# Optimization experiments

Measured on AMD Instinct MI355X. Metric: run time of the kernel, lower is better.

Reference implementation:

```python
import jax, jax.numpy as jnp
import numpy as np

B, T, N, F = 4096, 64, 8, 4
H = 64           # GRU hidden
EID = 16         # id embedding dim
CM = 32          # comm message dim
D = H + EID + CM # 112, attention dim
INV_SQRT_D = 1.0 / np.sqrt(112.0)


def setup_inputs() -> dict:
    key = jax.random.key(0)
    ks = jax.random.split(key, 24)
    def rn(k, shape, s=0.05):
        return jax.random.normal(k, shape, jnp.float32) * s
    return {
        "seq": jax.random.normal(ks[0], (B, T, N, F), jnp.float32),
        # GRU (torch layout: W_ih [3H,F], W_hh [3H,H], gates ordered r,z,n)
        "W_ih": rn(ks[1], (3 * H, F)), "W_hh": rn(ks[2], (3 * H, H)),
        "b_ih": rn(ks[3], (3 * H,)), "b_hh": rn(ks[4], (3 * H,)),
        "embed": rn(ks[5], (8, EID)),
        "Wm": rn(ks[6], (CM, H + EID)), "bm": rn(ks[7], (CM,)),
        "Wq": rn(ks[8], (D, D)), "bq": rn(ks[9], (D,)),
        "Wk": rn(ks[10], (D, D)), "bk": rn(ks[11], (D,)),
        "Wv": rn(ks[12], (D, D)), "bv": rn(ks[13], (D,)),
        "W1": rn(ks[14], (128, D)), "b1": rn(ks[15], (128,)),
        "W2": rn(ks[16], (128, 128)), "b2": rn(ks[17], (128,)),
        "Wmean": rn(ks[18], (2, 128)), "bmean": rn(ks[19], (2,)),
        "Wval": rn(ks[20], (1, 128)), "bval": rn(ks[21], (1,)),
    }


def _policy(seq, W_ih, W_hh, b_ih, b_hh, embed, Wm, bm,
            Wq, bq, Wk, bk, Wv, bv, W1, b1, W2, b2, Wmean, bmean, Wval, bval):
    Bb, Tt, Nn, Ff = seq.shape
    # Faithful to torch: raw view [B,T,N,F] -> [B*N,T,F] (no permute)
    x = seq.reshape(Bb * Nn, Tt, Ff)
    # Precompute all input-to-hidden projections once: [BN, T, 3H]
    x_proj = jnp.einsum('btf,gf->btg', x, W_ih) + b_ih

    def step(h, xp):
        gh = h @ W_hh.T + b_hh
        xr, xz, xn = jnp.split(xp, 3, axis=-1)
        hr, hz, hn = jnp.split(gh, 3, axis=-1)
        r = jax.nn.sigmoid(xr + hr)
        z = jax.nn.sigmoid(xz + hz)
        n = jnp.tanh(xn + r * hn)
        return (1.0 - z) * n + z * h, None

    h0 = jnp.zeros((Bb * Nn, H), seq.dtype)
    hT, _ = jax.lax.scan(step, h0, jnp.swapaxes(x_proj, 0, 1))  # carry == out[:, -1]
    h = hT.reshape(Bb, Nn, H)

    id_emb = jnp.broadcast_to(embed[:Nn], (Bb, Nn, EID))
    msgs = jnp.concatenate([h, id_emb], axis=-1) @ Wm.T + bm      # [B,N,32]
    c = jnp.broadcast_to(msgs.mean(axis=1, keepdims=True), (Bb, Nn, CM))
    h = jnp.concatenate([h, id_emb, c], axis=-1)                   # [B,N,112]

    Q = h @ Wq.T + bq
    K = h @ Wk.T + bk
    V = h @ Wv.T + bv
    attn = jax.nn.softmax(jnp.einsum('bnd,bmd->bnm', Q, K) * INV_SQRT_D, axis=-1)
    h = jnp.einsum('bnm,bmd->bnd', attn, V)

    h = jax.nn.relu(h @ W1.T + b1)
    h = jax.nn.relu(h @ W2.T + b2)
    return (h @ Wmean.T + bmean, h @ Wval.T + bval)


def reference(seq, W_ih, W_hh, b_ih, b_hh, embed, Wm, bm,
              Wq, bq, Wk, bk, Wv, bv, W1, b1, W2, b2, Wmean, bmean, Wval, bval):
    return _policy(seq, W_ih, W_hh, b_ih, b_hh, embed, Wm, bm,
                   Wq, bq, Wk, bk, Wv, bv, W1, b1, W2, b2,
                   Wmean, bmean, Wval, bval)
```

## Files before the change

### kernel.cpp

```cpp
#include <hip/hip_runtime.h>


typedef float f32x4 __attribute__((ext_vector_type(4)));
typedef short bf16x8 __attribute__((ext_vector_type(8)));

#define MFMA16 __builtin_amdgcn_mfma_f32_16x16x32_bf16
#define LOG2E 1.44269504088896f
#define INV_SQRT_D 0.09449111825230679f

__device__ __forceinline__ short f2bf(float f) {
    union { float f; unsigned u; } v; v.f = f;
    unsigned r = v.u + 0x7fffu + ((v.u >> 16) & 1u);
    return (short)(r >> 16);
}
__device__ __forceinline__ short f2bf_hu(float f) {
    union { float f; unsigned u; } v; v.f = f;
    return (short)((v.u + 0x8000u) >> 16);
}
__device__ __forceinline__ float fexp2(float x) { return __builtin_amdgcn_exp2f(x); }
__device__ __forceinline__ float frcp(float x)  { return __builtin_amdgcn_rcpf(x); }

__global__ void conv_kernel(
    const float* __restrict__ Wm, const float* __restrict__ Wq,
    const float* __restrict__ Wk, const float* __restrict__ Wv,
    const float* __restrict__ W1, const float* __restrict__ W2,
    const float* __restrict__ Wmean, const float* __restrict__ Wval,
    unsigned short* __restrict__ wf)
{
    int gid = blockIdx.x * 256 + threadIdx.x;
    if (gid >= 158 * 64) return;
    int fid = gid >> 6, lane = gid & 63;
    int l15 = lane & 15, q = lane >> 4;

    short out[8] = {0,0,0,0,0,0,0,0};
    if (fid < 154) {
        const float* W; int nrows, Klim, idx;
        if (fid < 6)        { W = Wm; nrows = 32;  Klim = 80;  idx = fid;       }
        else if (fid < 34)  { W = Wq; nrows = 112; Klim = 112; idx = fid - 6;   }
        else if (fid < 62)  { W = Wk; nrows = 112; Klim = 112; idx = fid - 34;  }
        else if (fid < 90)  { W = Wv; nrows = 112; Klim = 112; idx = fid - 62;  }
        else if (fid < 122) { W = W1; nrows = 128; Klim = 112; idx = fid - 90;  }
        else                { W = W2; nrows = 128; Klim = 128; idx = fid - 122; }
        int nch = (fid < 6) ? 3 : 4;
        int ct = idx / nch, ch = idx - ct * nch;
        int g = ct * 16 + l15, k0 = ch * 32 + q * 8;
        if (g < nrows && (k0 + 8) <= Klim) {
            const float* wp = W + (size_t)g * Klim + k0;
            #pragma unroll
            for (int u = 0; u < 8; ++u) out[u] = f2bf(wp[u]);
        }
    } else {
        int ch = fid - 154, k0 = ch * 32 + q * 8;
        const float* wp = (l15 == 0) ? Wmean : (l15 == 1) ? (Wmean + 128)
                          : (l15 == 2) ? Wval : nullptr;
        if (wp) {
            #pragma unroll
            for (int u = 0; u < 8; ++u) out[u] = f2bf(wp[k0 + u]);
        }
    }
    *(bf16x8*)(wf + ((size_t)fid * 64 + lane) * 8) = *(bf16x8*)out;
}

__global__ __launch_bounds__(256, 2) void gru_kernel(
    const float* __restrict__ seq,
    const float* __restrict__ W_ih,
    const float* __restrict__ W_hh,
    const float* __restrict__ b_ih,
    const float* __restrict__ b_hh,
    unsigned short* __restrict__ h_out)
{
    __shared__ short hlds[4][16][72];
    const int tid  = threadIdx.x;
    const int wave = tid >> 6;
    const int lane = tid & 63;
    const int l15  = lane & 15;
    const int q    = lane >> 4;
    const int seqbase = (blockIdx.x * 4 + wave) * 16;
    short (*hl)[72] = hlds[wave];

    {
        int* p = (int*)&hl[0][0];
        #pragma unroll
        for (int i = 0; i < 9; ++i) p[lane + 64 * i] = 0;
    }

    const float sc_rz = -LOG2E;
    const float sc_n  = 2.0f * LOG2E;

    bf16x8 Bh[12][2];
    bf16x8 B2[12];
    bf16x8 B2x[4];
    #pragma unroll
    for (int j = 0; j < 12; ++j) {
        int g = j * 16 + l15;
        float s = (j < 8) ? sc_rz : sc_n;
        #pragma unroll
        for (int c = 0; c < 2; ++c) {
            const float* wp = W_hh + g * 64 + c * 32 + q * 8;
            bf16x8 f;
            #pragma unroll
            for (int u = 0; u < 8; ++u) f[u] = f2bf(wp[u] * s);
            Bh[j][c] = f;
        }
        bf16x8 f2 = {0,0,0,0,0,0,0,0};
        if (q == 0) {
            if (j < 8) {
                #pragma unroll
                for (int u = 0; u < 4; ++u) f2[u] = f2bf(W_ih[g * 4 + u] * s);
                f2[4] = f2bf((b_ih[g] + b_hh[g]) * s);
            } else {
                f2[4] = f2bf(b_hh[g] * s);
            }
        }
        B2[j] = f2;
    }
    #pragma unroll
    for (int j2 = 0; j2 < 4; ++j2) {
        int g = 128 + j2 * 16 + l15;
        bf16x8 f = {0,0,0,0,0,0,0,0};
        if (q == 0) {
            #pragma unroll
            for (int u = 0; u < 4; ++u) f[u] = f2bf(W_ih[g * 4 + u] * sc_n);
            f[4] = f2bf(b_ih[g] * sc_n);
        }
        B2x[j2] = f;
    }

    const short onebf = 0x3f80;
    float h[4][4];
    #pragma unroll
    for (int j = 0; j < 4; ++j)
        #pragma unroll
        for (int r = 0; r < 4; ++r) h[j][r] = 0.f;

    f32x4 xc = *(const f32x4*)(seq + (size_t)(seqbase + l15) * 256);
    const f32x4 zz = {0.f, 0.f, 0.f, 0.f};

    for (int t = 0; t < 64; ++t) {
        f32x4 xnext;
        if (t < 63)
            xnext = *(const f32x4*)(seq + (size_t)(seqbase + l15) * 256 + (t + 1) * 4);

        bf16x8 A0 = *(const bf16x8*)&hl[l15][q * 8];
        bf16x8 A1 = *(const bf16x8*)&hl[l15][32 + q * 8];
        bf16x8 A2;
        A2[0] = f2bf_hu(xc[0]); A2[1] = f2bf_hu(xc[1]);
        A2[2] = f2bf_hu(xc[2]); A2[3] = f2bf_hu(xc[3]);
        A2[4] = onebf; A2[5] = 0; A2[6] = 0; A2[7] = 0;

        #pragma unroll
        for (int j = 0; j < 4; ++j) {
            f32x4 ar = MFMA16(A2, B2[j], zz, 0, 0, 0);
            ar = MFMA16(A0, Bh[j][0], ar, 0, 0, 0);
            ar = MFMA16(A1, Bh[j][1], ar, 0, 0, 0);
            f32x4 az = MFMA16(A2, B2[4 + j], zz, 0, 0, 0);
            az = MFMA16(A0, Bh[4 + j][0], az, 0, 0, 0);
            az = MFMA16(A1, Bh[4 + j][1], az, 0, 0, 0);
            f32x4 an = MFMA16(A2, B2[8 + j], zz, 0, 0, 0);
            an = MFMA16(A0, Bh[8 + j][0], an, 0, 0, 0);
            an = MFMA16(A1, Bh[8 + j][1], an, 0, 0, 0);
            f32x4 ax = MFMA16(A2, B2x[j], zz, 0, 0, 0);

            #pragma unroll
            for (int r = 0; r < 4; ++r) {
                float e_r  = fexp2(ar[r]);
                float rg   = frcp(1.f + e_r);
                float e_z  = fexp2(az[r]);
                float npre = fmaf(rg, an[r], ax[r]);
                float e_t  = fexp2(npre);
                float tp   = e_t + 1.f;
                float tm   = e_t - 1.f;
                float hv   = h[j][r];
                float num  = fmaf(hv, tp, e_z * tm);
                float den  = tp * (1.f + e_z);
                float hnew = num * frcp(den);
                h[j][r] = hnew;
                hl[q * 4 + r][16 * j + l15] = f2bf_hu(hnew);
            }
        }
        if (t < 63) xc = xnext;
    }

    #pragma unroll
    for (int j = 0; j < 4; ++j)
        #pragma unroll
        for (int r = 0; r < 4; ++r)
            h_out[(size_t)(seqbase + q * 4 + r) * 64 + 16 * j + l15] =
                (unsigned short)f2bf_hu(h[j][r]);
}

__global__ __launch_bounds__(256, 2) void head_kernel(
    const unsigned short* __restrict__ hseq,
    const unsigned short* __restrict__ wf,
    const float* __restrict__ embed,
    const float* __restrict__ bm, const float* __restrict__ bq,
    const float* __restrict__ bk, const float* __restrict__ bv,
    const float* __restrict__ b1, const float* __restrict__ b2,
    const float* __restrict__ bmean, const float* __restrict__ bval,
    float* __restrict__ out)
{
    __shared__ short R1[64][136];
    __shared__ short R2[64][136];
    __shared__ short R3[64][136];
    __shared__ short Vt[112][80];
    __shared__ short Pb[64][40];

    float (*msgs)[33]  = (float(*)[33])&R3[0][0];
    float (*cmean)[32] = (float(*)[32])&Pb[0][0];

    const int tid  = threadIdx.x;
    const int w    = tid >> 6;
    const int lane = tid & 63;
    const int l15  = lane & 15;
    const int q    = lane >> 4;
    const int agent0 = blockIdx.x * 64;
    const f32x4 zz4 = {0.f, 0.f, 0.f, 0.f};

    auto ld = [&](int fid) -> bf16x8 {
        return *(const bf16x8*)(wf + ((size_t)fid * 64 + lane) * 8);
    };

    {
        int* p;
        p = (int*)&R1[0][0]; for (int i = tid; i < 4352; i += 256) p[i] = 0;
        p = (int*)&R2[0][0]; for (int i = tid; i < 4352; i += 256) p[i] = 0;
        p = (int*)&Vt[0][0]; for (int i = tid; i < 4480; i += 256) p[i] = 0;
        p = (int*)&Pb[0][0]; for (int i = tid; i < 1280; i += 256) p[i] = 0;
    }
    __syncthreads();

    for (int i = tid; i < 512; i += 256) {
        int row = i >> 3, part = i & 7;
        *(bf16x8*)&R1[row][part * 8] =
            *(const bf16x8*)(hseq + (size_t)(agent0 + row) * 64 + part * 8);
    }
    for (int i = tid; i < 1024; i += 256) {
        int row = i >> 4, e = i & 15;
        R1[row][64 + e] = f2bf(embed[(row & 7) * 16 + e]);
    }
    __syncthreads();

    #pragma unroll
    for (int ct = 0; ct < 2; ++ct) {
        f32x4 acc = zz4;
        #pragma unroll
        for (int ch = 0; ch < 3; ++ch) {
            bf16x8 a = *(const bf16x8*)&R1[16 * w + l15][ch * 32 + q * 8];
            acc = MFMA16(a, ld(ct * 3 + ch), acc, 0, 0, 0);
        }
        float bias = bm[16 * ct + l15];
        #pragma unroll
        for (int r = 0; r < 4; ++r) msgs[16 * w + q * 4 + r][16 * ct + l15] = acc[r] + bias;
    }
    __syncthreads();

    {
        int b = tid >> 5, m = tid & 31;
        float s = 0.f;
        #pragma unroll
        for (int j = 0; j < 8; ++j) s += msgs[b * 8 + j][m];
        cmean[b][m] = 0.125f * s;
    }
    __syncthreads();
    for (int i = tid; i < 2048; i += 256) {
        int row = i >> 5, m = i & 31;
        R1[row][80 + m] = f2bf_hu(cmean[row >> 3][m]);
    }
    __syncthreads();

    for (int i = tid; i < 512; i += 256) {
        int row = i >> 3, cp = i & 7;
        *(int*)&R3[row][112 + cp * 2] = 0;
    }
    for (int i = tid; i < 768; i += 256) {
        int row = i / 12, cp = i - row * 12;
        *(int*)&Pb[row][16 + cp * 2] = 0;
    }
    #pragma unroll
    for (int ct = 0; ct < 7; ++ct) {
        f32x4 aq = zz4, ak = zz4, av = zz4;
        #pragma unroll
        for (int ch = 0; ch < 4; ++ch) {
            bf16x8 a = *(const bf16x8*)&R1[16 * w + l15][ch * 32 + q * 8];
            aq = MFMA16(a, ld(6  + ct * 4 + ch), aq, 0, 0, 0);
            ak = MFMA16(a, ld(34 + ct * 4 + ch), ak, 0, 0, 0);
            av = MFMA16(a, ld(62 + ct * 4 + ch), av, 0, 0, 0);
        }
        int col = 16 * ct + l15;
        float biq = bq[col], bik = bk[col], biv = bv[col];
        #pragma unroll
        for (int r = 0; r < 4; ++r) {
            int row = 16 * w + q * 4 + r;
            R2[row][col] = f2bf_hu((aq[r] + biq) * INV_SQRT_D);
            R3[row][col] = f2bf_hu(ak[r] + bik);
            Vt[col][row] = f2bf_hu(av[r] + biv);
        }
    }
    __syncthreads();

    {
        f32x4 acc = zz4;
        #pragma unroll
        for (int ch = 0; ch < 4; ++ch) {
            bf16x8 a = *(const bf16x8*)&R2[16 * w + l15][ch * 32 + q * 8];
            bf16x8 b = *(const bf16x8*)&R3[16 * w + l15][ch * 32 + q * 8];
            acc = MFMA16(a, b, acc, 0, 0, 0);
        }
        bool collow = (l15 < 8);
        #pragma unroll
        for (int r = 0; r < 4; ++r) {
            int rl = q * 4 + r;
            bool valid = ((rl < 8) == collow);
            float v = acc[r];
            float m = v;
            m = fmaxf(m, __shfl_xor(m, 1, 64));
            m = fmaxf(m, __shfl_xor(m, 2, 64));
            m = fmaxf(m, __shfl_xor(m, 4, 64));
            float e = fexp2(LOG2E * (v - m));
            float s = e;
            s += __shfl_xor(s, 1, 64);
            s += __shfl_xor(s, 2, 64);
            s += __shfl_xor(s, 4, 64);
            float pv = valid ? e * frcp(s) : 0.f;
            Pb[16 * w + rl][l15] = f2bf_hu(pv);
        }
    }
    __syncthreads();

    #pragma unroll
    for (int ct = 0; ct < 7; ++ct) {
        bf16x8 a = *(const bf16x8*)&Pb[16 * w + l15][q * 8];
        bf16x8 b = *(const bf16x8*)&Vt[16 * ct + l15][16 * w + q * 8];
        f32x4 acc = MFMA16(a, b, zz4, 0, 0, 0);
        #pragma unroll
        for (int r = 0; r < 4; ++r) R1[16 * w + q * 4 + r][16 * ct + l15] = f2bf_hu(acc[r]);
    }
    __syncthreads();

    #pragma unroll
    for (int ct = 0; ct < 8; ++ct) {
        f32x4 acc = zz4;
        #pragma unroll
        for (int ch = 0; ch < 4; ++ch) {
            bf16x8 a = *(const bf16x8*)&R1[16 * w + l15][ch * 32 + q * 8];
            acc = MFMA16(a, ld(90 + ct * 4 + ch), acc, 0, 0, 0);
        }
        float bias = b1[16 * ct + l15];
        #pragma unroll
        for (int r = 0; r < 4; ++r)
            R2[16 * w + q * 4 + r][16 * ct + l15] = f2bf_hu(fmaxf(acc[r] + bias, 0.f));
    }
    __syncthreads();

    #pragma unroll
    for (int ct = 0; ct < 8; ++ct) {
        f32x4 acc = zz4;
        #pragma unroll
        for (int ch = 0; ch < 4; ++ch) {
            bf16x8 a = *(const bf16x8*)&R2[16 * w + l15][ch * 32 + q * 8];
            acc = MFMA16(a, ld(122 + ct * 4 + ch), acc, 0, 0, 0);
        }
        float bias = b2[16 * ct + l15];
        #pragma unroll
        for (int r = 0; r < 4; ++r)
            R3[16 * w + q * 4 + r][16 * ct + l15] = f2bf_hu(fmaxf(acc[r] + bias, 0.f));
    }
    __syncthreads();

    {
        f32x4 acc = zz4;
        #pragma unroll
        for (int ch = 0; ch < 4; ++ch) {
            bf16x8 a = *(const bf16x8*)&R3[16 * w + l15][ch * 32 + q * 8];
            acc = MFMA16(a, ld(154 + ch), acc, 0, 0, 0);
        }
        if (l15 < 3) {
            float bias = (l15 == 0) ? bmean[0] : (l15 == 1) ? bmean[1] : bval[0];
            #pragma unroll
            for (int r = 0; r < 4; ++r) {
                int A = agent0 + 16 * w + q * 4 + r;
                float v = acc[r] + bias;
                if (l15 < 2) out[(size_t)A * 2 + l15] = v;
                else         out[65536 + A] = v;
            }
        }
    }
}

extern "C" void kernel_launch(void* const* d_in, const int* in_sizes, int n_in,
                              void* d_out, int out_size, void* d_ws, size_t ws_size,
                              hipStream_t stream) {
    const float* seq   = (const float*)d_in[0];
    const float* W_ih  = (const float*)d_in[1];
    const float* W_hh  = (const float*)d_in[2];
    const float* b_ih  = (const float*)d_in[3];
    const float* b_hh  = (const float*)d_in[4];
    const float* embed = (const float*)d_in[5];
    const float* Wm    = (const float*)d_in[6];
    const float* bm    = (const float*)d_in[7];
    const float* Wq    = (const float*)d_in[8];
    const float* bq    = (const float*)d_in[9];
    const float* Wk    = (const float*)d_in[10];
    const float* bk    = (const float*)d_in[11];
    const float* Wv    = (const float*)d_in[12];
    const float* bv    = (const float*)d_in[13];
    const float* W1    = (const float*)d_in[14];
    const float* b1    = (const float*)d_in[15];
    const float* W2    = (const float*)d_in[16];
    const float* b2    = (const float*)d_in[17];
    const float* Wmean = (const float*)d_in[18];
    const float* bmean = (const float*)d_in[19];
    const float* Wval  = (const float*)d_in[20];
    const float* bval  = (const float*)d_in[21];

    unsigned short* hbuf = (unsigned short*)d_ws;
    unsigned short* wf   = hbuf + (size_t)32768 * 64;

    conv_kernel<<<40, 256, 0, stream>>>(Wm, Wq, Wk, Wv, W1, W2, Wmean, Wval, wf);
    gru_kernel<<<512, 256, 0, stream>>>(seq, W_ih, W_hh, b_ih, b_hh, hbuf);
    head_kernel<<<512, 256, 0, stream>>>(hbuf, wf, embed, bm, bq, bk, bv,
                                         b1, b2, bmean, bval, (float*)d_out);
}
```

Baseline: 254.5 us.

## Fuse GRU and head into one per-wave kernel with LDS-only handoff

Merges the GRU recurrence and the attention/MLP head into a single kernel. Each wave keeps its 16 agents' final hidden state in its private LDS region and runs the head on them directly, which removes the global bf16 hidden-state round trip and one kernel launch. Block-wide __syncthreads are replaced by wave-local lgkmcnt waits, and the comm mean is computed with a shuffle reduction instead of a shared scratch pass. In exchange, per-block LDS grows, the head's weight-fragment loads now fall inside the long-latency GRU kernel, and the head work is serialized per wave after the recurrence.

```diff
diff --git a/kernel.cpp b/kernel.cpp
--- a/kernel.cpp
+++ b/kernel.cpp
@@ -19,6 +19,9 @@
 }
 __device__ __forceinline__ float fexp2(float x) { return __builtin_amdgcn_exp2f(x); }
 __device__ __forceinline__ float frcp(float x)  { return __builtin_amdgcn_rcpf(x); }
+__device__ __forceinline__ void lds_fence() {
+    __asm__ __volatile__("s_waitcnt lgkmcnt(0)" ::: "memory");
+}
 
 __global__ void conv_kernel(
     const float* __restrict__ Wm, const float* __restrict__ Wq,
@@ -50,7 +53,7 @@
             for (int u = 0; u < 8; ++u) out[u] = f2bf(wp[u]);
         }
     } else {
-        int ch = fid - 154, k0 = ch * 32 + q * 8;
+        int ch = fid - 154, k0 = ch * 32 + (lane >> 4) * 8;
         const float* wp = (l15 == 0) ? Wmean : (l15 == 1) ? (Wmean + 128)
                           : (l15 == 2) ? Wval : nullptr;
         if (wp) {
@@ -61,35 +64,56 @@
     *(bf16x8*)(wf + ((size_t)fid * 64 + lane) * 8) = *(bf16x8*)out;
 }
 
-__global__ __launch_bounds__(256, 2) void gru_kernel(
+__global__ __launch_bounds__(256, 2) void policy_kernel(
     const float* __restrict__ seq,
-    const float* __restrict__ W_ih,
-    const float* __restrict__ W_hh,
-    const float* __restrict__ b_ih,
-    const float* __restrict__ b_hh,
-    unsigned short* __restrict__ h_out)
+    const float* __restrict__ W_ih, const float* __restrict__ W_hh,
+    const float* __restrict__ b_ih, const float* __restrict__ b_hh,
+    const float* __restrict__ embed,
+    const unsigned short* __restrict__ wf,
+    const float* __restrict__ bm, const float* __restrict__ bq,
+    const float* __restrict__ bk, const float* __restrict__ bv,
+    const float* __restrict__ b1, const float* __restrict__ b2,
+    const float* __restrict__ bmean, const float* __restrict__ bval,
+    float* __restrict__ out)
 {
-    __shared__ short hlds[4][16][72];
+    __shared__ short R1s[4][16][136];
+    __shared__ short R2s[4][16][136];
+    __shared__ short R3s[4][16][136];
+    __shared__ short Vts[4][114][20];
+    __shared__ short Pbs[4][16][40];
+
     const int tid  = threadIdx.x;
-    const int wave = tid >> 6;
+    const int wv   = tid >> 6;
     const int lane = tid & 63;
     const int l15  = lane & 15;
     const int q    = lane >> 4;
-    const int seqbase = (blockIdx.x * 4 + wave) * 16;
-    short (*hl)[72] = hlds[wave];
-
-    {
-        int* p = (int*)&hl[0][0];
-        #pragma unroll
-        for (int i = 0; i < 9; ++i) p[lane + 64 * i] = 0;
+    const int seqbase = (blockIdx.x * 4 + wv) * 16;
+
+    short (*R1)[136] = R1s[wv];
+    short (*R2)[136] = R2s[wv];
+    short (*R3)[136] = R3s[wv];
+    short (*Vt)[20]  = Vts[wv];
+    short (*Pb)[40]  = Pbs[wv];
+    const f32x4 zz = {0.f, 0.f, 0.f, 0.f};
+
+    {
+        int* p;
+        p = (int*)&R1[0][0]; for (int i = lane; i < 1088; i += 64) p[i] = 0;
+        p = (int*)&R2[0][0]; for (int i = lane; i < 1088; i += 64) p[i] = 0;
+        p = (int*)&R3[0][0]; for (int i = lane; i < 1088; i += 64) p[i] = 0;
+        p = (int*)&Vt[0][0]; for (int i = lane; i < 1140; i += 64) p[i] = 0;
+        p = (int*)&Pb[0][0]; for (int i = lane; i < 320;  i += 64) p[i] = 0;
+    }
+    {
+        int row = lane >> 2, j0 = (lane & 3) * 4;
+        f32x4 e = *(const f32x4*)(embed + (row & 7) * 16 + j0);
+        #pragma unroll
+        for (int u = 0; u < 4; ++u) R1[row][64 + j0 + u] = f2bf(e[u]);
     }
 
     const float sc_rz = -LOG2E;
     const float sc_n  = 2.0f * LOG2E;
-
-    bf16x8 Bh[12][2];
-    bf16x8 B2[12];
-    bf16x8 B2x[4];
+    bf16x8 Bh[12][2], B2[12], B2x[4];
     #pragma unroll
     for (int j = 0; j < 12; ++j) {
         int g = j * 16 + l15;
@@ -125,6 +149,7 @@
         }
         B2x[j2] = f;
     }
+    lds_fence();
 
     const short onebf = 0x3f80;
     float h[4][4];
@@ -134,15 +159,14 @@
         for (int r = 0; r < 4; ++r) h[j][r] = 0.f;
 
     f32x4 xc = *(const f32x4*)(seq + (size_t)(seqbase + l15) * 256);
-    const f32x4 zz = {0.f, 0.f, 0.f, 0.f};
 
     for (int t = 0; t < 64; ++t) {
         f32x4 xnext;
         if (t < 63)
             xnext = *(const f32x4*)(seq + (size_t)(seqbase + l15) * 256 + (t + 1) * 4);
 
-        bf16x8 A0 = *(const bf16x8*)&hl[l15][q * 8];
-        bf16x8 A1 = *(const bf16x8*)&hl[l15][32 + q * 8];
+        bf16x8 A0 = *(const bf16x8*)&R1[l15][q * 8];
+        bf16x8 A1 = *(const bf16x8*)&R1[l15][32 + q * 8];
         bf16x8 A2;
         A2[0] = f2bf_hu(xc[0]); A2[1] = f2bf_hu(xc[1]);
         A2[2] = f2bf_hu(xc[2]); A2[3] = f2bf_hu(xc[3]);
@@ -175,113 +199,40 @@
                 float den  = tp * (1.f + e_z);
                 float hnew = num * frcp(den);
                 h[j][r] = hnew;
-                hl[q * 4 + r][16 * j + l15] = f2bf_hu(hnew);
+                R1[q * 4 + r][16 * j + l15] = f2bf_hu(hnew);
             }
         }
         if (t < 63) xc = xnext;
     }
-
-    #pragma unroll
-    for (int j = 0; j < 4; ++j)
-        #pragma unroll
-        for (int r = 0; r < 4; ++r)
-            h_out[(size_t)(seqbase + q * 4 + r) * 64 + 16 * j + l15] =
-                (unsigned short)f2bf_hu(h[j][r]);
-}
-
-__global__ __launch_bounds__(256, 2) void head_kernel(
-    const unsigned short* __restrict__ hseq,
-    const unsigned short* __restrict__ wf,
-    const float* __restrict__ embed,
-    const float* __restrict__ bm, const float* __restrict__ bq,
-    const float* __restrict__ bk, const float* __restrict__ bv,
-    const float* __restrict__ b1, const float* __restrict__ b2,
-    const float* __restrict__ bmean, const float* __restrict__ bval,
-    float* __restrict__ out)
-{
-    __shared__ short R1[64][136];
-    __shared__ short R2[64][136];
-    __shared__ short R3[64][136];
-    __shared__ short Vt[112][80];
-    __shared__ short Pb[64][40];
-
-    float (*msgs)[33]  = (float(*)[33])&R3[0][0];
-    float (*cmean)[32] = (float(*)[32])&Pb[0][0];
-
-    const int tid  = threadIdx.x;
-    const int w    = tid >> 6;
-    const int lane = tid & 63;
-    const int l15  = lane & 15;
-    const int q    = lane >> 4;
-    const int agent0 = blockIdx.x * 64;
-    const f32x4 zz4 = {0.f, 0.f, 0.f, 0.f};
+    lds_fence();
 
     auto ld = [&](int fid) -> bf16x8 {
         return *(const bf16x8*)(wf + ((size_t)fid * 64 + lane) * 8);
     };
 
-    {
-        int* p;
-        p = (int*)&R1[0][0]; for (int i = tid; i < 4352; i += 256) p[i] = 0;
-        p = (int*)&R2[0][0]; for (int i = tid; i < 4352; i += 256) p[i] = 0;
-        p = (int*)&Vt[0][0]; for (int i = tid; i < 4480; i += 256) p[i] = 0;
-        p = (int*)&Pb[0][0]; for (int i = tid; i < 1280; i += 256) p[i] = 0;
-    }
-    __syncthreads();
-
-    for (int i = tid; i < 512; i += 256) {
-        int row = i >> 3, part = i & 7;
-        *(bf16x8*)&R1[row][part * 8] =
-            *(const bf16x8*)(hseq + (size_t)(agent0 + row) * 64 + part * 8);
-    }
-    for (int i = tid; i < 1024; i += 256) {
-        int row = i >> 4, e = i & 15;
-        R1[row][64 + e] = f2bf(embed[(row & 7) * 16 + e]);
-    }
-    __syncthreads();
-
     #pragma unroll
     for (int ct = 0; ct < 2; ++ct) {
-        f32x4 acc = zz4;
+        f32x4 acc = zz;
         #pragma unroll
         for (int ch = 0; ch < 3; ++ch) {
-            bf16x8 a = *(const bf16x8*)&R1[16 * w + l15][ch * 32 + q * 8];
+            bf16x8 a = *(const bf16x8*)&R1[l15][ch * 32 + q * 8];
             acc = MFMA16(a, ld(ct * 3 + ch), acc, 0, 0, 0);
         }
-        float bias = bm[16 * ct + l15];
-        #pragma unroll
-        for (int r = 0; r < 4; ++r) msgs[16 * w + q * 4 + r][16 * ct + l15] = acc[r] + bias;
-    }
-    __syncthreads();
-
-    {
-        int b = tid >> 5, m = tid & 31;
-        float s = 0.f;
-        #pragma unroll
-        for (int j = 0; j < 8; ++j) s += msgs[b * 8 + j][m];
-        cmean[b][m] = 0.125f * s;
-    }
-    __syncthreads();
-    for (int i = tid; i < 2048; i += 256) {
-        int row = i >> 5, m = i & 31;
-        R1[row][80 + m] = f2bf_hu(cmean[row >> 3][m]);
-    }
-    __syncthreads();
-
-    for (int i = tid; i < 512; i += 256) {
-        int row = i >> 3, cp = i & 7;
-        *(int*)&R3[row][112 + cp * 2] = 0;
-    }
-    for (int i = tid; i < 768; i += 256) {
-        int row = i / 12, cp = i - row * 12;
-        *(int*)&Pb[row][16 + cp * 2] = 0;
-    }
+        float s = acc[0] + acc[1] + acc[2] + acc[3];
+        s += __shfl_xor(s, 16, 64);
+        float cv = 0.125f * s + bm[16 * ct + l15];
+        short cb = f2bf_hu(cv);
+        #pragma unroll
+        for (int r = 0; r < 4; ++r) R1[q * 4 + r][80 + 16 * ct + l15] = cb;
+    }
+    lds_fence();
+
     #pragma unroll
     for (int ct = 0; ct < 7; ++ct) {
-        f32x4 aq = zz4, ak = zz4, av = zz4;
-        #pragma unroll
-        for (int ch = 0; ch < 4; ++ch) {
-            bf16x8 a = *(const bf16x8*)&R1[16 * w + l15][ch * 32 + q * 8];
+        f32x4 aq = zz, ak = zz, av = zz;
+        #pragma unroll
+        for (int ch = 0; ch < 4; ++ch) {
+            bf16x8 a = *(const bf16x8*)&R1[l15][ch * 32 + q * 8];
             aq = MFMA16(a, ld(6  + ct * 4 + ch), aq, 0, 0, 0);
             ak = MFMA16(a, ld(34 + ct * 4 + ch), ak, 0, 0, 0);
             av = MFMA16(a, ld(62 + ct * 4 + ch), av, 0, 0, 0);
@@ -290,20 +241,20 @@
         float biq = bq[col], bik = bk[col], biv = bv[col];
         #pragma unroll
         for (int r = 0; r < 4; ++r) {
-            int row = 16 * w + q * 4 + r;
+            int row = q * 4 + r;
             R2[row][col] = f2bf_hu((aq[r] + biq) * INV_SQRT_D);
             R3[row][col] = f2bf_hu(ak[r] + bik);
             Vt[col][row] = f2bf_hu(av[r] + biv);
         }
     }
-    __syncthreads();
-
-    {
-        f32x4 acc = zz4;
-        #pragma unroll
-        for (int ch = 0; ch < 4; ++ch) {
-            bf16x8 a = *(const bf16x8*)&R2[16 * w + l15][ch * 32 + q * 8];
-            bf16x8 b = *(const bf16x8*)&R3[16 * w + l15][ch * 32 + q * 8];
+    lds_fence();
+
+    {
+        f32x4 acc = zz;
+        #pragma unroll
+        for (int ch = 0; ch < 4; ++ch) {
+            bf16x8 a = *(const bf16x8*)&R2[l15][ch * 32 + q * 8];
+            bf16x8 b = *(const bf16x8*)&R3[l15][ch * 32 + q * 8];
             acc = MFMA16(a, b, acc, 0, 0, 0);
         }
         bool collow = (l15 < 8);
@@ -322,63 +273,65 @@
             s += __shfl_xor(s, 2, 64);
             s += __shfl_xor(s, 4, 64);
             float pv = valid ? e * frcp(s) : 0.f;
-            Pb[16 * w + rl][l15] = f2bf_hu(pv);
-        }
-    }
-    __syncthreads();
-
-    #pragma unroll
-    for (int ct = 0; ct < 7; ++ct) {
-        bf16x8 a = *(const bf16x8*)&Pb[16 * w + l15][q * 8];
-        bf16x8 b = *(const bf16x8*)&Vt[16 * ct + l15][16 * w + q * 8];
-        f32x4 acc = MFMA16(a, b, zz4, 0, 0, 0);
-        #pragma unroll
-        for (int r = 0; r < 4; ++r) R1[16 * w + q * 4 + r][16 * ct + l15] = f2bf_hu(acc[r]);
-    }
-    __syncthreads();
+            Pb[rl][l15] = f2bf_hu(pv);
+        }
+    }
+    lds_fence();
+
+    {
+        bf16x8 a = *(const bf16x8*)&Pb[l15][q * 8];
+        #pragma unroll
+        for (int ct = 0; ct < 7; ++ct) {
+            bf16x8 b = *(const bf16x8*)&Vt[16 * ct + l15][q * 8];
+            f32x4 acc = MFMA16(a, b, zz, 0, 0, 0);
+            #pragma unroll
+            for (int r = 0; r < 4; ++r) R1[q * 4 + r][16 * ct + l15] = f2bf_hu(acc[r]);
+        }
+    }
+    lds_fence();
 
     #pragma unroll
     for (int ct = 0; ct < 8; ++ct) {
-        f32x4 acc = zz4;
-        #pragma unroll
-        for (int ch = 0; ch < 4; ++ch) {
-            bf16x8 a = *(const bf16x8*)&R1[16 * w + l15][ch * 32 + q * 8];
+        f32x4 acc = zz;
+        #pragma unroll
+        for (int ch = 0; ch < 4; ++ch) {
+            bf16x8 a = *(const bf16x8*)&R1[l15][ch * 32 + q * 8];
             acc = MFMA16(a, ld(90 + ct * 4 + ch), acc, 0, 0, 0);
         }
         float bias = b1[16 * ct + l15];
         #pragma unroll
         for (int r = 0; r < 4; ++r)
-            R2[16 * w + q * 4 + r][16 * ct + l15] = f2bf_hu(fmaxf(acc[r] + bias, 0.f));
-    }
-    __syncthreads();
+            R2[q * 4 + r][16 * ct + l15] = f2bf_hu(fmaxf(acc[r] + bias, 0.f));
+    }
+    lds_fence();
 
     #pragma unroll
     for (int ct = 0; ct < 8; ++ct) {
-        f32x4 acc = zz4;
-        #pragma unroll
-        for (int ch = 0; ch < 4; ++ch) {
-            bf16x8 a = *(const bf16x8*)&R2[16 * w + l15][ch * 32 + q * 8];
+        f32x4 acc = zz;
+        #pragma unroll
+        for (int ch = 0; ch < 4; ++ch) {
+            bf16x8 a = *(const bf16x8*)&R2[l15][ch * 32 + q * 8];
             acc = MFMA16(a, ld(122 + ct * 4 + ch), acc, 0, 0, 0);
         }
         float bias = b2[16 * ct + l15];
         #pragma unroll
         for (int r = 0; r < 4; ++r)
-            R3[16 * w + q * 4 + r][16 * ct + l15] = f2bf_hu(fmaxf(acc[r] + bias, 0.f));
-    }
-    __syncthreads();
-
-    {
-        f32x4 acc = zz4;
-        #pragma unroll
-        for (int ch = 0; ch < 4; ++ch) {
-            bf16x8 a = *(const bf16x8*)&R3[16 * w + l15][ch * 32 + q * 8];
+            R3[q * 4 + r][16 * ct + l15] = f2bf_hu(fmaxf(acc[r] + bias, 0.f));
+    }
+    lds_fence();
+
+    {
+        f32x4 acc = zz;
+        #pragma unroll
+        for (int ch = 0; ch < 4; ++ch) {
+            bf16x8 a = *(const bf16x8*)&R3[l15][ch * 32 + q * 8];
             acc = MFMA16(a, ld(154 + ch), acc, 0, 0, 0);
         }
         if (l15 < 3) {
             float bias = (l15 == 0) ? bmean[0] : (l15 == 1) ? bmean[1] : bval[0];
             #pragma unroll
             for (int r = 0; r < 4; ++r) {
-                int A = agent0 + 16 * w + q * 4 + r;
+                int A = seqbase + q * 4 + r;
                 float v = acc[r] + bias;
                 if (l15 < 2) out[(size_t)A * 2 + l15] = v;
                 else         out[65536 + A] = v;
@@ -413,11 +366,10 @@
     const float* Wval  = (const float*)d_in[20];
     const float* bval  = (const float*)d_in[21];
 
-    unsigned short* hbuf = (unsigned short*)d_ws;
-    unsigned short* wf   = hbuf + (size_t)32768 * 64;
+    unsigned short* wf = (unsigned short*)d_ws;
 
     conv_kernel<<<40, 256, 0, stream>>>(Wm, Wq, Wk, Wv, W1, W2, Wmean, Wval, wf);
-    gru_kernel<<<512, 256, 0, stream>>>(seq, W_ih, W_hh, b_ih, b_hh, hbuf);
-    head_kernel<<<512, 256, 0, stream>>>(hbuf, wf, embed, bm, bq, bk, bv,
-                                         b1, b2, bmean, bval, (float*)d_out);
-}
+    policy_kernel<<<512, 256, 0, stream>>>(seq, W_ih, W_hh, b_ih, b_hh, embed, wf,
+                                           bm, bq, bk, bv, b1, b2, bmean, bval,
+                                           (float*)d_out);
+}
```

Measured after the change: 249.0 us. 2.2% less time.
